# Kernel optimization log

Hardware: AMD Instinct MI355X
Metric: run time of the kernel (lower is better)

Reference implementation:

```python
import jax, jax.numpy as jnp
import numpy as np

H, HP, NH_M, NH_D = 1024, 64, 8, 8
B, T = 2, 2048
SPARSITY = 8
N_ROT = 32  # int(0.5 * HP), even
BASE = 10000.0


def _rope(x, pos, n_rot, base):
    # x: (..., L, d); pos: broadcastable to (..., L). Rotates first n_rot dims.
    half = n_rot // 2
    inv = base ** (-jnp.arange(half, dtype=x.dtype) / half)  # (half,)
    ang = pos[..., None] * inv                               # (..., L, half)
    cos, sin = jnp.cos(ang), jnp.sin(ang)
    x1, x2 = x[..., :half], x[..., half:n_rot]
    rot = jnp.concatenate([x1 * cos - x2 * sin, x1 * sin + x2 * cos], axis=-1)
    return jnp.concatenate([rot, x[..., n_rot:]], axis=-1)


def setup_inputs() -> dict:
    key = jax.random.key(0)
    ks = jax.random.split(key, 6)
    s = 0.02
    return {
        "X": jax.random.normal(ks[0], (B, T, H), jnp.float32),
        "mosa_router_w": jax.random.normal(ks[1], (H, NH_M), jnp.float32) * s,
        "mosa_wqkv": jax.random.normal(ks[2], (H, NH_M, 3 * HP), jnp.float32) * s,
        "mosa_wo": jax.random.normal(ks[3], (NH_M * HP, H), jnp.float32) * s,
        "dense_wqkv": jax.random.normal(ks[4], (H, NH_D, 3 * HP), jnp.float32) * s,
        "dense_wo": jax.random.normal(ks[5], (NH_D * HP, H), jnp.float32) * s,
    }


def _mosa_branch(X, router_w, wqkv, wo):
    # Expert-choice sparse attention: each head routes its own top-k tokens.
    b, t, _ = X.shape
    k = t // SPARSITY
    scores = jnp.einsum('bth,hn->bnt', X, router_w)                      # (b,nh,T)
    _, idx = jax.lax.top_k(scores, k)                                    # (b,nh,k)
    idx = jnp.sort(idx, axis=-1)                                         # keep temporal order
    gates = jax.nn.sigmoid(jnp.take_along_axis(scores, idx, axis=-1))    # (b,nh,k)
    Xg = jnp.take_along_axis(X[:, None], idx[..., None], axis=2)         # (b,nh,k,h)
    qkv = jnp.einsum('bnkh,hnd->bnkd', Xg, wqkv)                         # (b,nh,k,3hp)
    Q, K, V = jnp.split(qkv, 3, axis=-1)
    pos = idx.astype(X.dtype)                                            # original positions for RoPE
    Q = _rope(Q, pos, N_ROT, BASE)
    K = _rope(K, pos, N_ROT, BASE)
    att = jnp.einsum('bnqd,bnkd->bnqk', Q, K) / jnp.sqrt(jnp.asarray(HP, X.dtype))
    causal = idx[..., :, None] >= idx[..., None, :]                      # causality by original index
    att = jnp.where(causal, att, -jnp.inf)
    AV = jnp.einsum('bnqk,bnkd->bnqd', jax.nn.softmax(att, axis=-1), V)
    AV = AV * gates[..., None]
    # scatter selected-token outputs back to full sequence
    out = jnp.zeros((b, NH_M, t, HP), X.dtype)
    bi = jnp.arange(b)[:, None, None]
    hi = jnp.arange(NH_M)[None, :, None]
    out = out.at[bi, hi, idx].set(AV)                                    # (b,nh,T,hp)
    out = out.transpose(0, 2, 1, 3).reshape(b, t, NH_M * HP)
    return out @ wo


def _dense_branch(X, wqkv, wo):
    b, t, _ = X.shape
    qkv = jnp.einsum('bth,hnd->bntd', X, wqkv)                           # (b,nh,T,3hp)
    Q, K, V = jnp.split(qkv, 3, axis=-1)
    pos = jnp.arange(t, dtype=X.dtype)
    Q = _rope(Q, pos, N_ROT, BASE)
    K = _rope(K, pos, N_ROT, BASE)
    att = jnp.einsum('bnqd,bnkd->bnqk', Q, K) / jnp.sqrt(jnp.asarray(HP, X.dtype))
    causal = jnp.tril(jnp.ones((t, t), bool))
    att = jnp.where(causal, att, -jnp.inf)
    AV = jnp.einsum('bnqk,bnkd->bnqd', jax.nn.softmax(att, axis=-1), V)  # (b,nh,T,hp)
    return AV.transpose(0, 2, 1, 3).reshape(b, t, NH_D * HP) @ wo


def reference(X, mosa_router_w, mosa_wqkv, mosa_wo, dense_wqkv, dense_wo):
    return (_mosa_branch(X, mosa_router_w, mosa_wqkv, mosa_wo)
            + _dense_branch(X, dense_wqkv, dense_wo))
```

## Files before the change

kernel.cpp:

```cpp
#include <hip/hip_runtime.h>
#include <math.h>

constexpr int BB = 2;
constexpr int SEQ = 2048;
constexpr int HD = 1024;
constexpr int DH = 64;
constexpr int NHEAD = 8;
constexpr int D3 = 192;
constexpr int KSEL = 256;
constexpr float NEG = -1e30f;
constexpr float ROPE_C = -0.5756462732485115f;

typedef short short8 __attribute__((ext_vector_type(8)));
typedef float f32x4 __attribute__((ext_vector_type(4)));

__device__ __forceinline__ ushort bf16u(float f) {
  union { float f; unsigned u; } v; v.f = f;
  unsigned r = (v.u + 0x7FFFu + ((v.u >> 16) & 1u)) >> 16;
  return (ushort)r;
}
__device__ __forceinline__ float bf2f(ushort h) {
  union { unsigned u; float f; } v; v.u = ((unsigned)h) << 16;
  return v.f;
}

__device__ __forceinline__ void gl_lds16(const ushort* g, ushort* l) {
  __builtin_amdgcn_global_load_lds(
      (const __attribute__((address_space(1))) unsigned int*)g,
      (__attribute__((address_space(3))) unsigned int*)l, 16, 0, 0);
}

__device__ __forceinline__ unsigned long long rankkey(float s, int idx) {
  union { float f; unsigned u; } v; v.f = s;
  unsigned o = (v.u & 0x80000000u) ? ~v.u : (v.u | 0x80000000u);
  return ((unsigned long long)o << 11) | (unsigned)(2047 - idx);
}

__global__ __launch_bounds__(256) void cast_router(const float* __restrict__ X,
    const float* __restrict__ rw, ushort* __restrict__ Xb, float* __restrict__ scores) {
  __shared__ float rwT[8][8][132];
  int tid = threadIdx.x;
  for (int idx = tid; idx < 8192; idx += 256) {
    int h = idx & 1023, n = idx >> 10;
    rwT[n][h >> 7][h & 127] = rw[h * 8 + n];
  }
  __syncthreads();
  int row = blockIdx.x * 32 + (tid >> 3);
  int seg = tid & 7;
  const float* xrow = X + (size_t)row * HD + seg * 128;
  ushort* yrow = Xb + (size_t)row * HD + seg * 128;
  float acc[8] = {};
#pragma unroll 8
  for (int it = 0; it < 32; it++) {
    float4 xv = *(const float4*)(xrow + 4 * it);
    ushort4 cv;
    cv.x = bf16u(xv.x); cv.y = bf16u(xv.y); cv.z = bf16u(xv.z); cv.w = bf16u(xv.w);
    *(ushort4*)(yrow + 4 * it) = cv;
#pragma unroll
    for (int n = 0; n < 8; n++) {
      float4 rv = *(const float4*)&rwT[n][seg][4 * it];
      acc[n] += xv.x * rv.x + xv.y * rv.y + xv.z * rv.z + xv.w * rv.w;
    }
  }
#pragma unroll
  for (int n = 0; n < 8; n++) {
    acc[n] += __shfl_xor(acc[n], 1);
    acc[n] += __shfl_xor(acc[n], 2);
    acc[n] += __shfl_xor(acc[n], 4);
  }
  int b = row >> 11, t2 = row & (SEQ - 1);
  scores[((size_t)b * NHEAD + seg) * SEQ + t2] = acc[seg];
}

__global__ __launch_bounds__(256) void transpose_cast2(
    const float* __restrict__ W1, ushort* __restrict__ T1,
    const float* __restrict__ W2, ushort* __restrict__ T2, int K, int N) {
  const float* W = blockIdx.z ? W2 : W1;
  ushort* Wt = blockIdx.z ? T2 : T1;
  __shared__ float tile[32][33];
  int n0 = blockIdx.x * 32, k0 = blockIdx.y * 32;
  int tx = threadIdx.x & 31, ty = threadIdx.x >> 5;
#pragma unroll
  for (int i = 0; i < 4; i++)
    tile[ty + 8 * i][tx] = W[(size_t)(k0 + ty + 8 * i) * N + n0 + tx];
  __syncthreads();
#pragma unroll
  for (int i = 0; i < 4; i++)
    Wt[(size_t)(n0 + ty + 8 * i) * K + k0 + tx] = bf16u(tile[tx][ty + 8 * i]);
}

__global__ __launch_bounds__(256) void topk_partial(const float* __restrict__ scores,
    int* __restrict__ pranks) {
  int row = blockIdx.x;
  int c = blockIdx.y;
  __shared__ unsigned long long ck[128];
  const float* sp = scores + (size_t)row * SEQ;
  int tid = threadIdx.x;
  if (tid < 128) ck[tid] = rankkey(sp[c * 128 + tid], c * 128 + tid);
  __syncthreads();
  unsigned long long kv[8]; int p[8];
#pragma unroll
  for (int i = 0; i < 8; i++) {
    int vi = i * 256 + tid;
    kv[i] = rankkey(sp[vi], vi);
    p[i] = 0;
  }
#pragma unroll 8
  for (int j = 0; j < 128; j += 2) {
    unsigned long long k0 = ck[j], k1 = ck[j + 1];
#pragma unroll
    for (int i = 0; i < 8; i++) {
      p[i] += (k0 > kv[i]);
      p[i] += (k1 > kv[i]);
    }
  }
#pragma unroll
  for (int i = 0; i < 8; i++)
    pranks[((size_t)row * 16 + c) * SEQ + i * 256 + tid] = p[i];
}

__global__ __launch_bounds__(1024) void topk_select(const float* __restrict__ scores,
    const int* __restrict__ pranks, int* __restrict__ sel, float* __restrict__ gates) {
  int bn = blockIdx.x;
  __shared__ int wsum[16];
  int tid = threadIdx.x;
  int t0 = tid * 2;
  int r0 = 0, r1 = 0;
#pragma unroll
  for (int c = 0; c < 16; c++) {
    const int2 pp = *(const int2*)&pranks[((size_t)bn * 16 + c) * SEQ + t0];
    r0 += pp.x; r1 += pp.y;
  }
  int f0 = r0 < KSEL, f1 = r1 < KSEL;
  unsigned long long b0 = __ballot(f0), b1 = __ballot(f1);
  int lane = tid & 63, wv = tid >> 6;
  unsigned long long lower = (1ULL << lane) - 1ULL;
  int before = __popcll(b0 & lower) + __popcll(b1 & lower);
  int wtotal = __popcll(b0) + __popcll(b1);
  if (lane == 0) wsum[wv] = wtotal;
  __syncthreads();
  int woff = 0;
#pragma unroll
  for (int i2 = 0; i2 < 16; i2++) woff += (i2 < wv) ? wsum[i2] : 0;
  int base = woff + before;
  if (f0) { sel[bn * KSEL + base] = t0;
            gates[bn * KSEL + base] = 1.f / (1.f + __expf(-scores[(size_t)bn * SEQ + t0]));
            base++; }
  if (f1) { sel[bn * KSEL + base] = t0 + 1;
            gates[bn * KSEL + base] = 1.f / (1.f + __expf(-scores[(size_t)bn * SEQ + t0 + 1])); }
}

__global__ __launch_bounds__(256) void gemm_mosa_bf16(const ushort* __restrict__ Xb,
    const ushort* __restrict__ Wt, const int* __restrict__ sel,
    ushort* __restrict__ Qmg, ushort* __restrict__ Kmg, ushort* __restrict__ Vtmg) {
  __shared__ __align__(16) ushort As[64][40];
  __shared__ __align__(16) ushort Bs[64][40];
  int bn = blockIdx.x;
  int m0 = blockIdx.y * 64, n0 = blockIdx.z * 64;
  int b = bn >> 3, n = bn & 7;
  int tid = threadIdx.x;
  int lane = tid & 63, w = tid >> 6;
  int wm = w & 1, wn = w >> 1;
  int cc = lane & 15, quad = lane >> 4;
  int sr = tid >> 2, sc4 = tid & 3;

  int grow = sel[bn * KSEL + m0 + sr];
  const ushort* arow = Xb + ((size_t)(b * SEQ) + grow) * HD;
  const ushort* brow = Wt + ((size_t)(n * D3 + n0 + sr)) * HD;

  f32x4 acc[2][2];
#pragma unroll
  for (int i = 0; i < 2; i++)
#pragma unroll
    for (int j = 0; j < 2; j++)
#pragma unroll
      for (int r = 0; r < 4; r++) acc[i][j][r] = 0.f;

  for (int k0 = 0; k0 < HD; k0 += 32) {
    __syncthreads();
    *(short8*)&As[sr][8 * sc4] = *(const short8*)(arow + k0 + 8 * sc4);
    *(short8*)&Bs[sr][8 * sc4] = *(const short8*)(brow + k0 + 8 * sc4);
    __syncthreads();
    short8 af[2], bf_[2];
#pragma unroll
    for (int i = 0; i < 2; i++) af[i] = *(const short8*)&As[32 * wm + 16 * i + cc][8 * quad];
#pragma unroll
    for (int j = 0; j < 2; j++) bf_[j] = *(const short8*)&Bs[32 * wn + 16 * j + cc][8 * quad];
#pragma unroll
    for (int i = 0; i < 2; i++)
#pragma unroll
      for (int j = 0; j < 2; j++)
        acc[i][j] = __builtin_amdgcn_mfma_f32_16x16x32_bf16(af[i], bf_[j], acc[i][j], 0, 0, 0);
  }

  int bs = n0 + 32 * wn;
  if (bs == 0 || bs == 64) {
    float inv = __expf((float)cc * ROPE_C);
#pragma unroll
    for (int i = 0; i < 2; i++) {
      int row0 = m0 + 32 * wm + 16 * i + 4 * quad;
#pragma unroll
      for (int r = 0; r < 4; r++) {
        float pos = (float)sel[bn * KSEL + row0 + r];
        float ang = pos * inv;
        float cs = cosf(ang), sn = sinf(ang);
        float x1 = acc[i][0][r], x2 = acc[i][1][r];
        acc[i][0][r] = x1 * cs - x2 * sn;
        acc[i][1][r] = x1 * sn + x2 * cs;
      }
    }
  }

#pragma unroll
  for (int i = 0; i < 2; i++)
#pragma unroll
    for (int j = 0; j < 2; j++) {
      int col = bs + 16 * j + cc;
      int row0 = m0 + 32 * wm + 16 * i + 4 * quad;
      if (col < 64) {
#pragma unroll
        for (int r = 0; r < 4; r++)
          Qmg[((size_t)bn * KSEL + row0 + r) * 64 + col] = bf16u(acc[i][j][r] * 0.125f);
      } else if (col < 128) {
#pragma unroll
        for (int r = 0; r < 4; r++)
          Kmg[((size_t)bn * KSEL + row0 + r) * 64 + (col - 64)] = bf16u(acc[i][j][r]);
      } else {
        ushort4 pk;
        pk.x = bf16u(acc[i][j][0]); pk.y = bf16u(acc[i][j][1]);
        pk.z = bf16u(acc[i][j][2]); pk.w = bf16u(acc[i][j][3]);
        *(ushort4*)&Vtmg[((size_t)bn * 64 + (col - 128)) * KSEL + row0] = pk;
      }
    }
}

__global__ __launch_bounds__(256) void flash6(
    const ushort* __restrict__ Qg, const ushort* __restrict__ Kg,
    const ushort* __restrict__ Vtg,
    const ushort* __restrict__ Qmg, const ushort* __restrict__ Kmg,
    const ushort* __restrict__ Vtmg,
    const int* __restrict__ sel, const float* __restrict__ gates,
    ushort* __restrict__ Opart, float2* __restrict__ Mlp,
    ushort* __restrict__ avm) {
  __shared__ __align__(16) ushort Ks[2][64][64];
  __shared__ __align__(16) ushort Vt[2][64][64];
  __shared__ __align__(16) ushort Ps[64][64];

  int bx = blockIdx.x;
  bool mosa = bx >= 2048;
  int bn, qt, T, kstart, kstride;
  const ushort *Qb, *Kb, *Vb;
  if (!mosa) {
    bn = bx & 15; qt = (bx >> 4) & 31;
    kstart = bx >> 9; kstride = 4; T = SEQ;
    Qb = Qg + (size_t)bn * SEQ * 64;
    Kb = Kg + (size_t)bn * SEQ * 64;
    Vb = Vtg + (size_t)bn * 64 * SEQ;
  } else {
    int rr = bx - 2048;
    bn = rr & 15; qt = 3 - (rr >> 4);
    kstart = 0; kstride = 1; T = KSEL;
    Qb = Qmg + (size_t)bn * KSEL * 64;
    Kb = Kmg + (size_t)bn * KSEL * 64;
    Vb = Vtmg + (size_t)bn * 64 * KSEL;
  }
  int b = bn >> 3, n = bn & 7;
  int tid = threadIdx.x;
  int lane = tid & 63, w = tid >> 6;
  int cc = lane & 15, quad = lane >> 4;
  int qrow = 16 * w + cc;

  short8 bq[2];
  {
    const ushort* qsrc = Qb + (size_t)(qt * 64 + qrow) * 64;
    bq[0] = *(const short8*)(qsrc + 8 * quad);
    bq[1] = *(const short8*)(qsrc + 8 * (quad + 4));
  }

  int rloc = lane >> 3;
  int c_log = (lane & 7) ^ rloc;
  int row0 = 16 * w + rloc, row1 = row0 + 8;
  const ushort* pK0 = Kb + (size_t)row0 * 64 + 8 * c_log;
  const ushort* pK1 = Kb + (size_t)row1 * 64 + 8 * c_log;
  const ushort* pV0 = Vb + (size_t)row0 * T + 8 * c_log;
  const ushort* pV1 = Vb + (size_t)row1 * T + 8 * c_log;

  f32x4 oacc[4];
  float m = NEG, l = 0.f;
#pragma unroll
  for (int jd = 0; jd < 4; jd++)
#pragma unroll
    for (int r = 0; r < 4; r++) oacc[jd][r] = 0.f;

  if (kstart <= qt) {
    gl_lds16(pK0 + (size_t)kstart * 4096, &Ks[0][16 * w][0]);
    gl_lds16(pK1 + (size_t)kstart * 4096, &Ks[0][16 * w + 8][0]);
    gl_lds16(pV0 + kstart * 64, &Vt[0][16 * w][0]);
    gl_lds16(pV1 + kstart * 64, &Vt[0][16 * w + 8][0]);
  }

  int it = 0;
  for (int kt = kstart; kt <= qt; kt += kstride, it++) {
    int buf = it & 1;
    __syncthreads();
    int nk = kt + kstride;
    if (nk <= qt) {
      int nb = buf ^ 1;
      gl_lds16(pK0 + (size_t)nk * 4096, &Ks[nb][16 * w][0]);
      gl_lds16(pK1 + (size_t)nk * 4096, &Ks[nb][16 * w + 8][0]);
      gl_lds16(pV0 + nk * 64, &Vt[nb][16 * w][0]);
      gl_lds16(pV1 + nk * 64, &Vt[nb][16 * w + 8][0]);
    }

    f32x4 sacc[4];
#pragma unroll
    for (int j = 0; j < 4; j++)
#pragma unroll
      for (int r = 0; r < 4; r++) sacc[j][r] = 0.f;
#pragma unroll
    for (int ks = 0; ks < 2; ks++) {
#pragma unroll
      for (int j = 0; j < 4; j++) {
        int krow = 16 * j + cc;
        short8 ak = *(const short8*)&Ks[buf][krow][8 * ((quad + 4 * ks) ^ (krow & 7))];
        sacc[j] = __builtin_amdgcn_mfma_f32_16x16x32_bf16(ak, bq[ks], sacc[j], 0, 0, 0);
      }
    }
    if (kt == qt) {
#pragma unroll
      for (int j = 0; j < 4; j++)
#pragma unroll
        for (int r = 0; r < 4; r++)
          if (16 * j + 4 * quad + r > qrow) sacc[j][r] = NEG;
    }
    float mx = NEG;
#pragma unroll
    for (int j = 0; j < 4; j++)
#pragma unroll
      for (int r = 0; r < 4; r++) mx = fmaxf(mx, sacc[j][r]);
    mx = fmaxf(mx, __shfl_xor(mx, 16));
    mx = fmaxf(mx, __shfl_xor(mx, 32));
    float mn = fmaxf(m, mx);
    float sc = __expf(m - mn);
    m = mn;
    float rsum = 0.f;
    float p[4][4];
#pragma unroll
    for (int j = 0; j < 4; j++)
#pragma unroll
      for (int r = 0; r < 4; r++) { p[j][r] = __expf(sacc[j][r] - mn); rsum += p[j][r]; }
    rsum += __shfl_xor(rsum, 16);
    rsum += __shfl_xor(rsum, 32);
    l = l * sc + rsum;
#pragma unroll
    for (int j = 0; j < 4; j++) {
      ushort4 pk;
      pk.x = bf16u(p[j][0]); pk.y = bf16u(p[j][1]);
      pk.z = bf16u(p[j][2]); pk.w = bf16u(p[j][3]);
      int phys = (2 * j + (quad >> 1)) ^ (qrow & 7);
      *(ushort4*)&Ps[qrow][phys * 8 + 4 * (quad & 1)] = pk;
    }
#pragma unroll
    for (int r = 0; r < 4; r++) {
      float scr = __shfl(sc, 16 * quad + 4 * quad + r);
#pragma unroll
      for (int jd = 0; jd < 4; jd++) oacc[jd][r] *= scr;
    }
    __asm__ volatile("s_waitcnt lgkmcnt(0)" ::: "memory");
#pragma unroll
    for (int ks = 0; ks < 2; ks++) {
      short8 ap = *(const short8*)&Ps[qrow][8 * ((quad + 4 * ks) ^ (qrow & 7))];
#pragma unroll
      for (int jd = 0; jd < 4; jd++) {
        int vrow = 16 * jd + cc;
        short8 bv = *(const short8*)&Vt[buf][vrow][8 * ((quad + 4 * ks) ^ (vrow & 7))];
        oacc[jd] = __builtin_amdgcn_mfma_f32_16x16x32_bf16(ap, bv, oacc[jd], 0, 0, 0);
      }
    }
  }

  if (!mosa) {
    size_t pb = ((size_t)(bn * 32 + qt) * 4 + (size_t)(kstart));
    ushort* obase = Opart + pb * 4096;
#pragma unroll
    for (int r = 0; r < 4; r++) {
      int ql = 16 * w + 4 * quad + r;
#pragma unroll
      for (int jd = 0; jd < 4; jd++)
        obase[ql * 64 + 16 * jd + cc] = bf16u(oacc[jd][r]);
    }
    if (quad == 0) Mlp[pb * 64 + qrow] = make_float2(m, l);
  } else {
#pragma unroll
    for (int r = 0; r < 4; r++) {
      float lr = __shfl(l, 16 * quad + 4 * quad + r);
      int q = qt * 64 + 16 * w + 4 * quad + r;
      int trow = sel[bn * KSEL + q];
      float scale = gates[bn * KSEL + q] / lr;
      size_t row = (size_t)(b * SEQ + trow);
      ushort* orow = avm + row * (NHEAD * DH) + n * DH;
#pragma unroll
      for (int jd = 0; jd < 4; jd++)
        orow[16 * jd + cc] = bf16u(oacc[jd][r] * scale);
    }
  }
}

__global__ __launch_bounds__(256) void flash_merge(const ushort* __restrict__ Opart,
    const float2* __restrict__ Mlp, ushort* __restrict__ avd) {
  int bq = blockIdx.x;
  int bn = bq >> 5, qt = bq & 31;
  int b = bn >> 3, n = bn & 7;
  int tid = threadIdx.x;
  int q = tid >> 2, ds = (tid & 3) * 16;
  size_t pb = (size_t)bq * 4;
  float2 ml[4];
#pragma unroll
  for (int c = 0; c < 4; c++) ml[c] = Mlp[(pb + c) * 64 + q];
  float M = fmaxf(fmaxf(ml[0].x, ml[1].x), fmaxf(ml[2].x, ml[3].x));
  float wgt[4], L = 0.f;
#pragma unroll
  for (int c = 0; c < 4; c++) { wgt[c] = __expf(ml[c].x - M); L += wgt[c] * ml[c].y; }
  float inv = 1.f / L;
  float acc[16] = {};
#pragma unroll
  for (int c = 0; c < 4; c++) {
    const ushort* op = Opart + (pb + c) * 4096 + q * 64 + ds;
#pragma unroll
    for (int d = 0; d < 16; d++) acc[d] += wgt[c] * bf2f(op[d]);
  }
  ushort* orow = avd + ((size_t)(b * SEQ + qt * 64 + q)) * (NHEAD * DH) + n * DH + ds;
#pragma unroll
  for (int d = 0; d < 16; d++) orow[d] = bf16u(acc[d] * inv);
}

template <int MODE>
__global__ __launch_bounds__(256) void gemm_bf16(
    const ushort* __restrict__ A1, const ushort* __restrict__ B1t, int K1,
    const ushort* __restrict__ A2, const ushort* __restrict__ B2t, int K2,
    void* __restrict__ outv, int N,
    ushort* __restrict__ Qo, ushort* __restrict__ Ko, ushort* __restrict__ Vto) {
  __shared__ __align__(16) ushort As[128][32];
  __shared__ __align__(16) ushort Bs[128][32];
  int m0 = blockIdx.x * 128, n0 = blockIdx.y * 128;
  int tid = threadIdx.x;
  int lane = tid & 63, wave = tid >> 6;
  int wm = wave & 1, wn = wave >> 1;
  int cc = lane & 15, quad = lane >> 4;

  int srow = 16 * wave + (lane >> 2);
  int c_log = ((lane & 3) - (lane >> 3)) & 3;

  f32x4 acc[4][4];
#pragma unroll
  for (int i = 0; i < 4; i++)
#pragma unroll
    for (int j = 0; j < 4; j++)
#pragma unroll
      for (int r = 0; r < 4; r++) acc[i][j][r] = 0.f;

  const int npass = (MODE == 0) ? 2 : 1;
  for (int pass = 0; pass < npass; pass++) {
    const ushort* A = pass ? A2 : A1;
    const ushort* Bt = pass ? B2t : B1t;
    int K = pass ? K2 : K1;
    const ushort* pA0 = A + (size_t)(m0 + srow) * K + 8 * c_log;
    const ushort* pA1 = A + (size_t)(m0 + srow + 64) * K + 8 * c_log;
    const ushort* pB0 = Bt + (size_t)(n0 + srow) * K + 8 * c_log;
    const ushort* pB1 = Bt + (size_t)(n0 + srow + 64) * K + 8 * c_log;
    for (int k0 = 0; k0 < K; k0 += 32) {
      __syncthreads();
      gl_lds16(pA0 + k0, &As[16 * wave][0]);
      gl_lds16(pA1 + k0, &As[16 * wave + 64][0]);
      gl_lds16(pB0 + k0, &Bs[16 * wave][0]);
      gl_lds16(pB1 + k0, &Bs[16 * wave + 64][0]);
      __syncthreads();
      short8 af[4], bfr[4];
#pragma unroll
      for (int i = 0; i < 4; i++) {
        int ra = 64 * wm + 16 * i + cc;
        af[i] = *(const short8*)&As[ra][8 * ((quad + (ra >> 1)) & 3)];
      }
#pragma unroll
      for (int j = 0; j < 4; j++) {
        int rb = 64 * wn + 16 * j + cc;
        bfr[j] = *(const short8*)&Bs[rb][8 * ((quad + (rb >> 1)) & 3)];
      }
#pragma unroll
      for (int i = 0; i < 4; i++)
#pragma unroll
        for (int j = 0; j < 4; j++)
          acc[i][j] = __builtin_amdgcn_mfma_f32_16x16x32_bf16(af[i], bfr[j], acc[i][j], 0, 0, 0);
    }
  }

  if (MODE == 1) {
    int bs = (n0 + 64 * wn) % 192;
    if (bs < 128) {
      float inv = __expf((float)cc * ROPE_C);
#pragma unroll
      for (int i = 0; i < 4; i++) {
        int row0 = m0 + 64 * wm + 16 * i + 4 * quad;
#pragma unroll
        for (int r = 0; r < 4; r++) {
          float pos = (float)((row0 + r) & (SEQ - 1));
          float ang = pos * inv;
          float cs = cosf(ang), sn = sinf(ang);
          float x1 = acc[i][0][r], x2 = acc[i][1][r];
          acc[i][0][r] = x1 * cs - x2 * sn;
          acc[i][1][r] = x1 * sn + x2 * cs;
        }
      }
    }
  }

#pragma unroll
  for (int i = 0; i < 4; i++) {
#pragma unroll
    for (int j = 0; j < 4; j++) {
      int colg = n0 + 64 * wn + 16 * j + cc;
      int row0 = m0 + 64 * wm + 16 * i + 4 * quad;
      if (MODE == 0) {
#pragma unroll
        for (int r = 0; r < 4; r++)
          ((float*)outv)[(size_t)(row0 + r) * N + colg] = acc[i][j][r];
      } else {
        int nn = colg / 192, c = colg % 192;
        int b2 = row0 >> 11, t2 = row0 & 2047;
        int bn2 = b2 * 8 + nn;
        if (c < 64) {
#pragma unroll
          for (int r = 0; r < 4; r++)
            Qo[((size_t)bn2 * SEQ + t2 + r) * 64 + c] = bf16u(acc[i][j][r] * 0.125f);
        } else if (c < 128) {
#pragma unroll
          for (int r = 0; r < 4; r++)
            Ko[((size_t)bn2 * SEQ + t2 + r) * 64 + (c - 64)] = bf16u(acc[i][j][r]);
        } else {
          ushort4 pk;
          pk.x = bf16u(acc[i][j][0]); pk.y = bf16u(acc[i][j][1]);
          pk.z = bf16u(acc[i][j][2]); pk.w = bf16u(acc[i][j][3]);
          *(ushort4*)&Vto[((size_t)bn2 * 64 + (c - 128)) * SEQ + t2] = pk;
        }
      }
    }
  }
}

extern "C" void kernel_launch(void* const* d_in, const int* in_sizes, int n_in,
                              void* d_out, int out_size, void* d_ws, size_t ws_size,
                              hipStream_t stream) {
  const float* X          = (const float*)d_in[0];
  const float* router_w   = (const float*)d_in[1];
  const float* mosa_wqkv  = (const float*)d_in[2];
  const float* mosa_wo    = (const float*)d_in[3];
  const float* dense_wqkv = (const float*)d_in[4];
  const float* dense_wo   = (const float*)d_in[5];
  float* out = (float*)d_out;
  char* ws = (char*)d_ws;

  float*  scores  = (float*) (ws + 0);
  int*    sel     = (int*)   (ws + 131072);
  float*  gates   = (float*) (ws + 147456);
  ushort* avm     = (ushort*)(ws + 163840);
  ushort* avd     = (ushort*)(ws + 4358144);
  ushort* Xb      = (ushort*)(ws + 8552448);
  ushort* Wqkv_t  = (ushort*)(ws + 16941056);
  ushort* Wmq_t   = (ushort*)(ws + 20086784);
  ushort* Wdo_t   = (ushort*)(ws + 23232512);
  ushort* Wmo_t   = (ushort*)(ws + 24281088);
  ushort* Qg      = (ushort*)(ws + 25329664);
  ushort* Kg      = (ushort*)(ws + 29523968);
  ushort* Vtg     = (ushort*)(ws + 33718272);
  ushort* Qmg     = (ushort*)(ws + 37912576);
  ushort* Kmg     = (ushort*)(ws + 38436864);
  ushort* Vtmg    = (ushort*)(ws + 38961152);
  int*    pranks  = (int*)   (ws + 39485440);
  ushort* Opart   = (ushort*)(ws + 41582592);
  float2* Mlp     = (float2*)(ws + 58359808);

  hipMemsetAsync(avm, 0, (size_t)BB * SEQ * NHEAD * DH * sizeof(ushort), stream);

  cast_router<<<BB * SEQ / 32, 256, 0, stream>>>(X, router_w, Xb, scores);
  transpose_cast2<<<dim3(48, 32, 2), 256, 0, stream>>>(dense_wqkv, Wqkv_t,
                                                       mosa_wqkv, Wmq_t, 1024, 1536);
  transpose_cast2<<<dim3(32, 16, 2), 256, 0, stream>>>(dense_wo, Wdo_t,
                                                       mosa_wo, Wmo_t, 512, 1024);

  topk_partial<<<dim3(BB * NHEAD, 16), 256, 0, stream>>>(scores, pranks);
  topk_select<<<BB * NHEAD, 1024, 0, stream>>>(scores, pranks, sel, gates);

  gemm_mosa_bf16<<<dim3(BB * NHEAD, KSEL / 64, D3 / 64), 256, 0, stream>>>(
      Xb, Wmq_t, sel, Qmg, Kmg, Vtmg);
  gemm_bf16<1><<<dim3(32, 12), 256, 0, stream>>>(Xb, Wqkv_t, 1024,
      (const ushort*)nullptr, (const ushort*)nullptr, 0, nullptr, NHEAD * D3,
      Qg, Kg, Vtg);

  flash6<<<2112, 256, 0, stream>>>(Qg, Kg, Vtg, Qmg, Kmg, Vtmg, sel, gates,
                                   Opart, Mlp, avm);
  flash_merge<<<512, 256, 0, stream>>>(Opart, Mlp, avd);

  gemm_bf16<0><<<dim3(32, 8), 256, 0, stream>>>(avm, Wmo_t, 512, avd, Wdo_t, 512, out, HD,
                                                nullptr, nullptr, nullptr);
}
```

Before: 224.8 us.

## Fuse memset and weight transposes, halve QKV GEMM M-tile, vectorize merge loads

Zeroing of the MoSA output buffer moves into cast_router, and the two transpose-cast launches become a single four-way launch, cutting the launch count. The dense QKV GEMM uses a 64-row M tile, doubling its grid from 384 to 768 blocks to fill more CUs. flash_merge now reads its bf16 partials with 16-byte vector loads. The cost is more B-tile reloads per output in the QKV GEMM and some idle blocks in the padded transpose grid.

```diff
diff --git a/kernel.cpp b/kernel.cpp
--- a/kernel.cpp
+++ b/kernel.cpp
@@ -37,9 +37,17 @@
 }
 
 __global__ __launch_bounds__(256) void cast_router(const float* __restrict__ X,
-    const float* __restrict__ rw, ushort* __restrict__ Xb, float* __restrict__ scores) {
+    const float* __restrict__ rw, ushort* __restrict__ Xb, float* __restrict__ scores,
+    ushort* __restrict__ avm) {
   __shared__ float rwT[8][8][132];
   int tid = threadIdx.x;
+  {
+    uint4* az = (uint4*)avm;
+    int gid = blockIdx.x * 256 + tid;
+    uint4 z = make_uint4(0, 0, 0, 0);
+#pragma unroll
+    for (int i = 0; i < 8; i++) az[gid + 32768 * i] = z;
+  }
   for (int idx = tid; idx < 8192; idx += 256) {
     int h = idx & 1023, n = idx >> 10;
     rwT[n][h >> 7][h & 127] = rw[h * 8 + n];
@@ -72,13 +80,20 @@
   scores[((size_t)b * NHEAD + seg) * SEQ + t2] = acc[seg];
 }
 
-__global__ __launch_bounds__(256) void transpose_cast2(
+__global__ __launch_bounds__(256) void transpose_cast4(
+    const float* __restrict__ W0, ushort* __restrict__ T0,
     const float* __restrict__ W1, ushort* __restrict__ T1,
-    const float* __restrict__ W2, ushort* __restrict__ T2, int K, int N) {
-  const float* W = blockIdx.z ? W2 : W1;
-  ushort* Wt = blockIdx.z ? T2 : T1;
+    const float* __restrict__ W2, ushort* __restrict__ T2,
+    const float* __restrict__ W3, ushort* __restrict__ T3) {
+  int z = blockIdx.z;
+  const float* W; ushort* Wt; int K, N;
+  if (z == 0)      { W = W0; Wt = T0; K = 1024; N = 1536; }
+  else if (z == 1) { W = W1; Wt = T1; K = 1024; N = 1536; }
+  else if (z == 2) { W = W2; Wt = T2; K = 512;  N = 1024; }
+  else             { W = W3; Wt = T3; K = 512;  N = 1024; }
+  int n0 = blockIdx.x * 32, k0 = blockIdx.y * 32;
+  if (n0 >= N || k0 >= K) return;
   __shared__ float tile[32][33];
-  int n0 = blockIdx.x * 32, k0 = blockIdx.y * 32;
   int tx = threadIdx.x & 31, ty = threadIdx.x >> 5;
 #pragma unroll
   for (int i = 0; i < 4; i++)
@@ -426,8 +441,12 @@
 #pragma unroll
   for (int c = 0; c < 4; c++) {
     const ushort* op = Opart + (pb + c) * 4096 + q * 64 + ds;
-#pragma unroll
-    for (int d = 0; d < 16; d++) acc[d] += wgt[c] * bf2f(op[d]);
+    short8 v0 = *(const short8*)op;
+    short8 v1 = *(const short8*)(op + 8);
+#pragma unroll
+    for (int d = 0; d < 8; d++) acc[d] += wgt[c] * bf2f(((const ushort*)&v0)[d]);
+#pragma unroll
+    for (int d = 0; d < 8; d++) acc[8 + d] += wgt[c] * bf2f(((const ushort*)&v1)[d]);
   }
   ushort* orow = avd + ((size_t)(b * SEQ + qt * 64 + q)) * (NHEAD * DH) + n * DH + ds;
 #pragma unroll
@@ -440,9 +459,11 @@
     const ushort* __restrict__ A2, const ushort* __restrict__ B2t, int K2,
     void* __restrict__ outv, int N,
     ushort* __restrict__ Qo, ushort* __restrict__ Ko, ushort* __restrict__ Vto) {
-  __shared__ __align__(16) ushort As[128][32];
+  constexpr int TM = (MODE == 1) ? 64 : 128;
+  constexpr int WI = TM / 32;
+  __shared__ __align__(16) ushort As[TM][32];
   __shared__ __align__(16) ushort Bs[128][32];
-  int m0 = blockIdx.x * 128, n0 = blockIdx.y * 128;
+  int m0 = blockIdx.x * TM, n0 = blockIdx.y * 128;
   int tid = threadIdx.x;
   int lane = tid & 63, wave = tid >> 6;
   int wm = wave & 1, wn = wave >> 1;
@@ -451,9 +472,9 @@
   int srow = 16 * wave + (lane >> 2);
   int c_log = ((lane & 3) - (lane >> 3)) & 3;
 
-  f32x4 acc[4][4];
-#pragma unroll
-  for (int i = 0; i < 4; i++)
+  f32x4 acc[WI][4];
+#pragma unroll
+  for (int i = 0; i < WI; i++)
 #pragma unroll
     for (int j = 0; j < 4; j++)
 #pragma unroll
@@ -465,20 +486,20 @@
     const ushort* Bt = pass ? B2t : B1t;
     int K = pass ? K2 : K1;
     const ushort* pA0 = A + (size_t)(m0 + srow) * K + 8 * c_log;
-    const ushort* pA1 = A + (size_t)(m0 + srow + 64) * K + 8 * c_log;
+    const ushort* pA1 = A + (size_t)(m0 + srow + (TM == 128 ? 64 : 0)) * K + 8 * c_log;
     const ushort* pB0 = Bt + (size_t)(n0 + srow) * K + 8 * c_log;
     const ushort* pB1 = Bt + (size_t)(n0 + srow + 64) * K + 8 * c_log;
     for (int k0 = 0; k0 < K; k0 += 32) {
       __syncthreads();
       gl_lds16(pA0 + k0, &As[16 * wave][0]);
-      gl_lds16(pA1 + k0, &As[16 * wave + 64][0]);
+      if (TM == 128) gl_lds16(pA1 + k0, &As[(16 * wave + 64) % TM][0]);
       gl_lds16(pB0 + k0, &Bs[16 * wave][0]);
       gl_lds16(pB1 + k0, &Bs[16 * wave + 64][0]);
       __syncthreads();
-      short8 af[4], bfr[4];
-#pragma unroll
-      for (int i = 0; i < 4; i++) {
-        int ra = 64 * wm + 16 * i + cc;
+      short8 af[WI], bfr[4];
+#pragma unroll
+      for (int i = 0; i < WI; i++) {
+        int ra = (TM / 2) * wm + 16 * i + cc;
         af[i] = *(const short8*)&As[ra][8 * ((quad + (ra >> 1)) & 3)];
       }
 #pragma unroll
@@ -487,7 +508,7 @@
         bfr[j] = *(const short8*)&Bs[rb][8 * ((quad + (rb >> 1)) & 3)];
       }
 #pragma unroll
-      for (int i = 0; i < 4; i++)
+      for (int i = 0; i < WI; i++)
 #pragma unroll
         for (int j = 0; j < 4; j++)
           acc[i][j] = __builtin_amdgcn_mfma_f32_16x16x32_bf16(af[i], bfr[j], acc[i][j], 0, 0, 0);
@@ -499,8 +520,8 @@
     if (bs < 128) {
       float inv = __expf((float)cc * ROPE_C);
 #pragma unroll
-      for (int i = 0; i < 4; i++) {
-        int row0 = m0 + 64 * wm + 16 * i + 4 * quad;
+      for (int i = 0; i < WI; i++) {
+        int row0 = m0 + (TM / 2) * wm + 16 * i + 4 * quad;
 #pragma unroll
         for (int r = 0; r < 4; r++) {
           float pos = (float)((row0 + r) & (SEQ - 1));
@@ -515,11 +536,11 @@
   }
 
 #pragma unroll
-  for (int i = 0; i < 4; i++) {
+  for (int i = 0; i < WI; i++) {
 #pragma unroll
     for (int j = 0; j < 4; j++) {
       int colg = n0 + 64 * wn + 16 * j + cc;
-      int row0 = m0 + 64 * wm + 16 * i + 4 * quad;
+      int row0 = m0 + (TM / 2) * wm + 16 * i + 4 * quad;
       if (MODE == 0) {
 #pragma unroll
         for (int r = 0; r < 4; r++)
@@ -579,20 +600,16 @@
   ushort* Opart   = (ushort*)(ws + 41582592);
   float2* Mlp     = (float2*)(ws + 58359808);
 
-  hipMemsetAsync(avm, 0, (size_t)BB * SEQ * NHEAD * DH * sizeof(ushort), stream);
-
-  cast_router<<<BB * SEQ / 32, 256, 0, stream>>>(X, router_w, Xb, scores);
-  transpose_cast2<<<dim3(48, 32, 2), 256, 0, stream>>>(dense_wqkv, Wqkv_t,
-                                                       mosa_wqkv, Wmq_t, 1024, 1536);
-  transpose_cast2<<<dim3(32, 16, 2), 256, 0, stream>>>(dense_wo, Wdo_t,
-                                                       mosa_wo, Wmo_t, 512, 1024);
+  cast_router<<<BB * SEQ / 32, 256, 0, stream>>>(X, router_w, Xb, scores, avm);
+  transpose_cast4<<<dim3(48, 32, 4), 256, 0, stream>>>(
+      dense_wqkv, Wqkv_t, mosa_wqkv, Wmq_t, dense_wo, Wdo_t, mosa_wo, Wmo_t);
 
   topk_partial<<<dim3(BB * NHEAD, 16), 256, 0, stream>>>(scores, pranks);
   topk_select<<<BB * NHEAD, 1024, 0, stream>>>(scores, pranks, sel, gates);
 
   gemm_mosa_bf16<<<dim3(BB * NHEAD, KSEL / 64, D3 / 64), 256, 0, stream>>>(
       Xb, Wmq_t, sel, Qmg, Kmg, Vtmg);
-  gemm_bf16<1><<<dim3(32, 12), 256, 0, stream>>>(Xb, Wqkv_t, 1024,
+  gemm_bf16<1><<<dim3(64, 12), 256, 0, stream>>>(Xb, Wqkv_t, 1024,
       (const ushort*)nullptr, (const ushort*)nullptr, 0, nullptr, NHEAD * D3,
       Qg, Kg, Vtg);
 
```

New measurement: 213.9 us. -4.9%, faster.
